# Performance work log

Hardware: AMD Instinct MI355X
Metric: run time of the kernel (lower is better)

Reference implementation:

```python
import jax, jax.numpy as jnp
import numpy as np

D_IN = 1024
D_OUT = 1024
NUM_HEADS = 16
HEAD_DIM = D_OUT // NUM_HEADS


def setup_inputs() -> dict:
    key = jax.random.key(0)
    ks = jax.random.split(key, 6)
    B, S = 2, 2048
    x = jax.random.normal(ks[0], (B, S, D_IN), dtype=jnp.float32)
    # nn.Linear stores weight as [out, in]; y = x @ W.T
    scale_in = 1.0 / np.sqrt(D_IN)
    w_query = jax.random.uniform(ks[1], (D_OUT, D_IN), jnp.float32, -scale_in, scale_in)
    w_key = jax.random.uniform(ks[2], (D_OUT, D_IN), jnp.float32, -scale_in, scale_in)
    w_value = jax.random.uniform(ks[3], (D_OUT, D_IN), jnp.float32, -scale_in, scale_in)
    scale_out = 1.0 / np.sqrt(D_OUT)
    w_out = jax.random.uniform(ks[4], (D_OUT, D_OUT), jnp.float32, -scale_out, scale_out)
    b_out = jax.random.uniform(ks[5], (D_OUT,), jnp.float32, -scale_out, scale_out)
    return {"x": x, "w_query": w_query, "w_key": w_key, "w_value": w_value,
            "w_out": w_out, "b_out": b_out}


def reference(x, w_query, w_key, w_value, w_out, b_out):
    B, S, _ = x.shape
    H, Dh = NUM_HEADS, HEAD_DIM
    # projections (no qkv bias), split heads -> [B, H, S, Dh]
    q = (x @ w_query.T).reshape(B, S, H, Dh).transpose(0, 2, 1, 3)
    k = (x @ w_key.T).reshape(B, S, H, Dh).transpose(0, 2, 1, 3)
    v = (x @ w_value.T).reshape(B, S, H, Dh).transpose(0, 2, 1, 3)
    # explicit [B, H, S, S] scores with causal mask (matches masked_fill(triu,-inf))
    scores = jnp.einsum('bhqd,bhkd->bhqk', q, k)
    causal = jnp.tril(jnp.ones((S, S), dtype=bool))  # True = keep
    scores = jnp.where(causal, scores, -jnp.inf)
    attn = jax.nn.softmax(scores / np.sqrt(Dh).astype(np.float32), axis=-1)
    # dropout p=0.0 -> identity
    ctx = jnp.einsum('bhqk,bhkd->bhqd', attn, v)  # [B, H, S, Dh]
    ctx = ctx.transpose(0, 2, 1, 3).reshape(B, S, H * Dh)
    return ctx @ w_out.T + b_out
```

## Files before the change

### kernel.cpp

```cpp
#include <hip/hip_runtime.h>
#include <hip/hip_bf16.h>

typedef __attribute__((ext_vector_type(8))) short short8;
typedef __attribute__((ext_vector_type(4))) short short4_t;
typedef __attribute__((ext_vector_type(8))) float f32x8;
typedef __attribute__((ext_vector_type(4))) float f32x4;
typedef __attribute__((ext_vector_type(2))) unsigned uint2v;
typedef __attribute__((ext_vector_type(4))) unsigned uint4v;

#define MFMA16(a, b, c) __builtin_amdgcn_mfma_f32_16x16x32_bf16((a), (b), (c), 0, 0, 0)


static __device__ __forceinline__ short f2bf(float f) {
    __hip_bfloat16 h = __float2bfloat16(f);
    return *reinterpret_cast<short*>(&h);
}

static __device__ __forceinline__ unsigned pack2bf(float lo, float hi) {
    return ((unsigned)f2bf(lo) & 0xffffu) | ((unsigned)f2bf(hi) << 16);
}

static __device__ __forceinline__ short8 u4_to_s8(uint4v u) {
    short8 s;
    __builtin_memcpy(&s, &u, 16);
    return s;
}

static __device__ __forceinline__ void g2l16(const void* g, void* l) {
    __builtin_amdgcn_global_load_lds(
        (const __attribute__((address_space(1))) void*)g,
        (__attribute__((address_space(3))) void*)l,
        16, 0, 0);
}

__global__ __launch_bounds__(256) void cvt_kernel(
    const float* __restrict__ x,  const float* __restrict__ wq,
    const float* __restrict__ wk, const float* __restrict__ wv,
    const float* __restrict__ wo, __hip_bfloat16* __restrict__ ws)
{
    const size_t e = ((size_t)blockIdx.x * 256 + threadIdx.x) * 8;
    const float* src;
    __hip_bfloat16* dst;
    size_t off;
    if (e < 4194304)      { src = x;  dst = ws + 16777216; off = e; }
    else if (e < 5242880) { src = wq; dst = ws + 20971520; off = e - 4194304; }
    else if (e < 6291456) { src = wk; dst = ws + 20971520 + 1048576; off = e - 5242880; }
    else if (e < 7340032) { src = wv; dst = ws + 20971520 + 2097152; off = e - 6291456; }
    else                  { src = wo; dst = ws + 24117248; off = e - 7340032; }

    f32x8 v = *reinterpret_cast<const f32x8*>(src + off);
    short8 o;
#pragma unroll
    for (int j = 0; j < 8; ++j) o[j] = f2bf(v[j]);
    *reinterpret_cast<short8*>(reinterpret_cast<short*>(dst) + off) = o;
}

__global__ __launch_bounds__(256) void qkv_gemm_kernel(
    const __hip_bfloat16* __restrict__ xbf_,
    const __hip_bfloat16* __restrict__ wqkv_,
    __hip_bfloat16* __restrict__ qkv_out)
{
    const int bid = blockIdx.x;
    const int xcd = bid & 7, kb = bid >> 3;
    const int mBlk = xcd * 4 + (kb / 24);
    const int nBlk = kb % 24;

    const int tid  = threadIdx.x;
    const int lane = tid & 63;
    const int wid  = tid >> 6;
    const int l16  = lane & 15;
    const int lhi  = lane >> 4;
    const int wr = wid >> 1, wc = wid & 1;

    const short* A = reinterpret_cast<const short*>(xbf_);
    const short* Bm = reinterpret_cast<const short*>(wqkv_);
    const int r0A = mBlk * 128, r0B = nBlk * 128;

    __shared__ __align__(16) short sA[128 * 64];
    __shared__ __align__(16) short sB[128 * 64];

    f32x4 acc[4][4] = {};

    for (int kk = 0; kk < 1024; kk += 64) {
#pragma unroll
        for (int it = 0; it < 4; ++it) {
            const int G = it * 256 + tid;
            const int row = G >> 3, gs = G & 7;
            const int gl = gs ^ (row & 7);
            short* lp = sA + (size_t)(it * 256 + wid * 64) * 8;
            g2l16(A + (size_t)(r0A + row) * 1024 + kk + gl * 8, lp);
        }
#pragma unroll
        for (int it = 0; it < 4; ++it) {
            const int G = it * 256 + tid;
            const int row = G >> 3, gs = G & 7;
            const int gl = gs ^ (row & 7);
            short* lp = sB + (size_t)(it * 256 + wid * 64) * 8;
            g2l16(Bm + (size_t)(r0B + row) * 1024 + kk + gl * 8, lp);
        }
        __syncthreads();

#pragma unroll
        for (int ks = 0; ks < 2; ++ks) {
            short8 a[4], b[4];
#pragma unroll
            for (int i = 0; i < 4; ++i) {
                const int row = wr * 64 + i * 16 + l16;
                const int sg = (ks * 4 + lhi) ^ (row & 7);
                a[i] = *reinterpret_cast<const short8*>(&sA[row * 64 + sg * 8]);
            }
#pragma unroll
            for (int j = 0; j < 4; ++j) {
                const int row = wc * 64 + j * 16 + l16;
                const int sg = (ks * 4 + lhi) ^ (row & 7);
                b[j] = *reinterpret_cast<const short8*>(&sB[row * 64 + sg * 8]);
            }
#pragma unroll
            for (int i = 0; i < 4; ++i)
#pragma unroll
                for (int j = 0; j < 4; ++j)
                    acc[i][j] = MFMA16(a[i], b[j], acc[i][j]);
        }
        __syncthreads();
    }

    const int nTileBase = nBlk * 128 + wc * 64;
    const int mat = (nTileBase >> 10);
    __hip_bfloat16* dst = qkv_out + (size_t)mat * 4194304;
    const int mBase = r0A + wr * 64;

    if (mat < 2) {
        const float qscl = (mat == 0) ? 0.18033688f : 1.0f;
#pragma unroll
        for (int i = 0; i < 4; ++i)
#pragma unroll
            for (int j = 0; j < 4; ++j)
#pragma unroll
                for (int r = 0; r < 4; ++r) {
                    const int mRow = mBase + i * 16 + lhi * 4 + r;
                    const int nCol = (nTileBase + j * 16 + l16) & 1023;
                    const int bb = mRow >> 11, s = mRow & 2047;
                    const int h = nCol >> 6, d = nCol & 63;
                    dst[(((size_t)(bb * 16 + h) * 2048 + s) << 6) + d] =
                        __float2bfloat16(acc[i][j][r] * qscl);
                }
    } else {
#pragma unroll
        for (int i = 0; i < 4; ++i) {
            const int mRow0 = mBase + i * 16 + lhi * 4;
            const int bb = mRow0 >> 11, s0 = mRow0 & 2047;
#pragma unroll
            for (int j = 0; j < 4; ++j) {
                const int nCol = (nTileBase + j * 16 + l16) & 1023;
                const int h = nCol >> 6, d = nCol & 63;
                short4_t v4;
#pragma unroll
                for (int r = 0; r < 4; ++r) v4[r] = f2bf(acc[i][j][r]);
                *reinterpret_cast<short4_t*>(
                    reinterpret_cast<short*>(dst) +
                    (((size_t)(bb * 16 + h) * 64 + d) << 11) + s0) = v4;
            }
        }
    }
}

__global__ __launch_bounds__(256, 4) void attn_kernel(
    const __hip_bfloat16* __restrict__ qkv,
    __hip_bfloat16* __restrict__ ctx)
{
    const int tid  = threadIdx.x;
    const int lane = tid & 63;
    const int wid  = tid >> 6;
    const int l16 = lane & 15;
    const int lhi = lane >> 4;

    const int bid = blockIdx.x;
    const int xcd = bid & 7, idx = bid >> 3;
    const int h4 = idx & 3, tg = idx >> 2;
    const int bh = xcd * 4 + h4;
    const int g  = (tg < 16) ? (31 - tg) : (tg - 16);
    const int qt = g * 4 + wid;
    const int q0 = qt * 16;
    const int ns_blk = g + 1;

    const short* Q  = reinterpret_cast<const short*>(qkv) + (size_t)bh * 131072;
    const short* K  = Q + 4194304;
    const short* Vt = Q + 8388608;

    __shared__ __align__(16) short sK[2][64 * 64];
    __shared__ __align__(16) short sV[2][64 * 64];

    const int bb = bh >> 4, h = bh & 15;
    const int qrow = q0 + l16;
    const int r7 = l16 & 7;

    short8 qf[2];
    qf[0] = *reinterpret_cast<const short8*>(Q + (size_t)qrow * 64 + lhi * 8);
    qf[1] = *reinterpret_cast<const short8*>(Q + (size_t)qrow * 64 + 32 + lhi * 8);

    f32x4 oacc[4] = {};
    float lsum = 0.0f;

    auto stage = [&](int buf, int kv0) {
#pragma unroll
        for (int it = 0; it < 2; ++it) {
            const int G = it * 256 + tid;
            const int row = G >> 3, gs = G & 7;
            const int gl = gs ^ (row & 7);
            g2l16(K + (size_t)(kv0 + row) * 64 + gl * 8, &sK[buf][(size_t)G * 8]);
            g2l16(Vt + (size_t)row * 2048 + kv0 + gl * 8, &sV[buf][(size_t)G * 8]);
        }
    };

    stage(0, 0);
    asm volatile("s_waitcnt vmcnt(0)" ::: "memory");
    __syncthreads();

    int cur = 0;
#pragma unroll 1
    for (int st = 0; st < ns_blk; ++st) {
        const int kv0 = st * 64;
        if (st + 1 < ns_blk) stage(cur ^ 1, kv0 + 64);

        f32x4 sc[4];
#pragma unroll
        for (int nt = 0; nt < 4; ++nt) {
            f32x4 s = {};
#pragma unroll
            for (int ks = 0; ks < 2; ++ks) {
                const int sg = (ks * 4 + lhi) ^ r7;
                short8 kb = *reinterpret_cast<const short8*>(
                    &sK[cur][(nt * 16 + l16) * 64 + sg * 8]);
                s = MFMA16(kb, qf[ks], s);
            }
            sc[nt] = s;
        }

        if (st == ns_blk - 1) {
#pragma unroll
            for (int nt = 0; nt < 4; ++nt) {
                const int kvb = kv0 + nt * 16 + lhi * 4;
#pragma unroll
                for (int r = 0; r < 4; ++r)
                    if (kvb + r > qrow) sc[nt][r] = -1.0e38f;
            }
        }

        unsigned pw[4][2];
#pragma unroll
        for (int nt = 0; nt < 4; ++nt) {
            const float p0 = exp2f(sc[nt][0]);
            const float p1 = exp2f(sc[nt][1]);
            const float p2 = exp2f(sc[nt][2]);
            const float p3 = exp2f(sc[nt][3]);
            lsum += (p0 + p1) + (p2 + p3);
            pw[nt][0] = pack2bf(p0, p1);
            pw[nt][1] = pack2bf(p2, p3);
        }

#pragma unroll
        for (int ks = 0; ks < 2; ++ks) {
            uint4v up;
            up[0] = pw[2 * ks][0];
            up[1] = pw[2 * ks][1];
            up[2] = pw[2 * ks + 1][0];
            up[3] = pw[2 * ks + 1][1];
            short8 pa = u4_to_s8(up);
#pragma unroll
            for (int dt = 0; dt < 4; ++dt) {
                const int row = dt * 16 + l16;
                const int g0 = (ks * 4 + (lhi >> 1)) ^ (row & 7);
                const int g1 = (ks * 4 + 2 + (lhi >> 1)) ^ (row & 7);
                const int sub = (lhi & 1) * 8;
                const char* base = reinterpret_cast<const char*>(&sV[cur][row * 64]);
                uint2v lo  = *reinterpret_cast<const uint2v*>(base + g0 * 16 + sub);
                uint2v hiw = *reinterpret_cast<const uint2v*>(base + g1 * 16 + sub);
                uint4v uv;
                uv[0] = lo[0];  uv[1] = lo[1];
                uv[2] = hiw[0]; uv[3] = hiw[1];
                short8 vb = u4_to_s8(uv);
                oacc[dt] = MFMA16(pa, vb, oacc[dt]);
            }
        }

        asm volatile("s_waitcnt vmcnt(0)" ::: "memory");
        __syncthreads();
        cur ^= 1;
    }

    float rs = lsum;
    rs += __shfl_xor(rs, 16);
    rs += __shfl_xor(rs, 32);
    const float rinvq = 1.0f / rs;
    float rinv[4];
#pragma unroll
    for (int r = 0; r < 4; ++r) rinv[r] = __shfl(rinvq, lhi * 4 + r);

#pragma unroll
    for (int dt = 0; dt < 4; ++dt)
#pragma unroll
        for (int r = 0; r < 4; ++r) {
            const int q = q0 + lhi * 4 + r;
            ctx[((size_t)bb * 2048 + q) * 1024 + h * 64 + dt * 16 + l16] =
                __float2bfloat16(oacc[dt][r] * rinv[r]);
        }
}

__global__ __launch_bounds__(256) void out_gemm_kernel(
    const __hip_bfloat16* __restrict__ ctx,
    const __hip_bfloat16* __restrict__ wobf,
    const float* __restrict__ bo,
    float* __restrict__ out)
{
    const int bid = blockIdx.x;
    const int xcd = bid & 7, kb = bid >> 3;
    const int mBlk = xcd * 4 + (kb >> 3);
    const int nBlk = kb & 7;

    const int tid  = threadIdx.x;
    const int lane = tid & 63;
    const int wid  = tid >> 6;
    const int l16  = lane & 15;
    const int lhi  = lane >> 4;
    const int wr = wid >> 1, wc = wid & 1;

    const short* A = reinterpret_cast<const short*>(ctx);
    const short* Bm = reinterpret_cast<const short*>(wobf);
    const int r0A = mBlk * 128, r0B = nBlk * 128;

    __shared__ __align__(16) short sA[128 * 64];
    __shared__ __align__(16) short sB[128 * 64];

    f32x4 acc[4][4] = {};

    for (int kk = 0; kk < 1024; kk += 64) {
#pragma unroll
        for (int it = 0; it < 4; ++it) {
            const int G = it * 256 + tid;
            const int row = G >> 3, gs = G & 7;
            const int gl = gs ^ (row & 7);
            short* lp = sA + (size_t)(it * 256 + wid * 64) * 8;
            g2l16(A + (size_t)(r0A + row) * 1024 + kk + gl * 8, lp);
        }
#pragma unroll
        for (int it = 0; it < 4; ++it) {
            const int G = it * 256 + tid;
            const int row = G >> 3, gs = G & 7;
            const int gl = gs ^ (row & 7);
            short* lp = sB + (size_t)(it * 256 + wid * 64) * 8;
            g2l16(Bm + (size_t)(r0B + row) * 1024 + kk + gl * 8, lp);
        }
        __syncthreads();

#pragma unroll
        for (int ks = 0; ks < 2; ++ks) {
            short8 a[4], b[4];
#pragma unroll
            for (int i = 0; i < 4; ++i) {
                const int row = wr * 64 + i * 16 + l16;
                const int sg = (ks * 4 + lhi) ^ (row & 7);
                a[i] = *reinterpret_cast<const short8*>(&sA[row * 64 + sg * 8]);
            }
#pragma unroll
            for (int j = 0; j < 4; ++j) {
                const int row = wc * 64 + j * 16 + l16;
                const int sg = (ks * 4 + lhi) ^ (row & 7);
                b[j] = *reinterpret_cast<const short8*>(&sB[row * 64 + sg * 8]);
            }
#pragma unroll
            for (int i = 0; i < 4; ++i)
#pragma unroll
                for (int j = 0; j < 4; ++j)
                    acc[i][j] = MFMA16(a[i], b[j], acc[i][j]);
        }
        __syncthreads();
    }

    const int mBase = r0A + wr * 64;
    const int nBase = r0B + wc * 64;
#pragma unroll
    for (int i = 0; i < 4; ++i)
#pragma unroll
        for (int j = 0; j < 4; ++j)
#pragma unroll
            for (int r = 0; r < 4; ++r) {
                const int mRow = mBase + i * 16 + lhi * 4 + r;
                const int nCol = nBase + j * 16 + l16;
                out[(size_t)mRow * 1024 + nCol] = acc[i][j][r] + bo[nCol];
            }
}

extern "C" void kernel_launch(void* const* d_in, const int* in_sizes, int n_in,
                              void* d_out, int out_size, void* d_ws, size_t ws_size,
                              hipStream_t stream) {
    const float* x  = (const float*)d_in[0];
    const float* wq = (const float*)d_in[1];
    const float* wk = (const float*)d_in[2];
    const float* wv = (const float*)d_in[3];
    const float* wo = (const float*)d_in[4];
    const float* bo = (const float*)d_in[5];

    __hip_bfloat16* ws = (__hip_bfloat16*)d_ws;
    __hip_bfloat16* ctx  = ws + 12582912;
    __hip_bfloat16* xbf  = ws + 16777216;
    __hip_bfloat16* wqkv = ws + 20971520;
    __hip_bfloat16* wobf = ws + 24117248;
    float* out = (float*)d_out;

    cvt_kernel<<<4096, 256, 0, stream>>>(x, wq, wk, wv, wo, ws);
    qkv_gemm_kernel<<<768, 256, 0, stream>>>(xbf, wqkv, ws);
    attn_kernel<<<1024, 256, 0, stream>>>(ws, ctx);
    out_gemm_kernel<<<256, 256, 0, stream>>>(ctx, wobf, bo, out);
}
```

Before: 118.3 us.

## Process two query tiles per wave in attention and vectorize Q/K stores

The attention kernel now gives each wave 32 query rows (two 16-row tiles) instead of 16, so every K/V tile staged in LDS and every fragment read from LDS feeds twice as many MFMAs. Block count is halved to 512 and the occupancy hint drops to 3. Waves whose rows end before the block's last KV tile skip that tile's compute. Separately, the QKV GEMM swaps MFMA operand order for the Q/K outputs so each lane holds 4 contiguous head-dim values and can write them as one 8-byte store instead of scalar stores. The cost is higher register pressure and fewer blocks to balance across CUs.

```diff
diff --git a/kernel.cpp b/kernel.cpp
--- a/kernel.cpp
+++ b/kernel.cpp
@@ -76,6 +76,10 @@
     const short* Bm = reinterpret_cast<const short*>(wqkv_);
     const int r0A = mBlk * 128, r0B = nBlk * 128;
 
+    const int nTileBase = nBlk * 128 + wc * 64;
+    const int mat = (nTileBase >> 10);
+    const bool swp = (mat < 2);
+
     __shared__ __align__(16) short sA[128 * 64];
     __shared__ __align__(16) short sB[128 * 64];
 
@@ -115,35 +119,44 @@
                 const int sg = (ks * 4 + lhi) ^ (row & 7);
                 b[j] = *reinterpret_cast<const short8*>(&sB[row * 64 + sg * 8]);
             }
-#pragma unroll
-            for (int i = 0; i < 4; ++i)
-#pragma unroll
-                for (int j = 0; j < 4; ++j)
-                    acc[i][j] = MFMA16(a[i], b[j], acc[i][j]);
+            if (swp) {
+#pragma unroll
+                for (int i = 0; i < 4; ++i)
+#pragma unroll
+                    for (int j = 0; j < 4; ++j)
+                        acc[i][j] = MFMA16(b[j], a[i], acc[i][j]);
+            } else {
+#pragma unroll
+                for (int i = 0; i < 4; ++i)
+#pragma unroll
+                    for (int j = 0; j < 4; ++j)
+                        acc[i][j] = MFMA16(a[i], b[j], acc[i][j]);
+            }
         }
         __syncthreads();
     }
 
-    const int nTileBase = nBlk * 128 + wc * 64;
-    const int mat = (nTileBase >> 10);
     __hip_bfloat16* dst = qkv_out + (size_t)mat * 4194304;
     const int mBase = r0A + wr * 64;
 
-    if (mat < 2) {
+    if (swp) {
         const float qscl = (mat == 0) ? 0.18033688f : 1.0f;
 #pragma unroll
-        for (int i = 0; i < 4; ++i)
-#pragma unroll
-            for (int j = 0; j < 4; ++j)
-#pragma unroll
-                for (int r = 0; r < 4; ++r) {
-                    const int mRow = mBase + i * 16 + lhi * 4 + r;
-                    const int nCol = (nTileBase + j * 16 + l16) & 1023;
-                    const int bb = mRow >> 11, s = mRow & 2047;
-                    const int h = nCol >> 6, d = nCol & 63;
-                    dst[(((size_t)(bb * 16 + h) * 2048 + s) << 6) + d] =
-                        __float2bfloat16(acc[i][j][r] * qscl);
-                }
+        for (int i = 0; i < 4; ++i) {
+            const int mRow = mBase + i * 16 + l16;
+            const int bb = mRow >> 11, s = mRow & 2047;
+#pragma unroll
+            for (int j = 0; j < 4; ++j) {
+                const int nCol0 = (nTileBase + j * 16 + lhi * 4) & 1023;
+                const int h = nCol0 >> 6, d0 = nCol0 & 63;
+                short4_t v4;
+#pragma unroll
+                for (int r = 0; r < 4; ++r) v4[r] = f2bf(acc[i][j][r] * qscl);
+                *reinterpret_cast<short4_t*>(
+                    reinterpret_cast<short*>(dst) +
+                    (((size_t)(bb * 16 + h) * 2048 + s) << 6) + d0) = v4;
+            }
+        }
     } else {
 #pragma unroll
         for (int i = 0; i < 4; ++i) {
@@ -164,7 +177,7 @@
     }
 }
 
-__global__ __launch_bounds__(256, 4) void attn_kernel(
+__global__ __launch_bounds__(256, 3) void attn_kernel(
     const __hip_bfloat16* __restrict__ qkv,
     __hip_bfloat16* __restrict__ ctx)
 {
@@ -178,10 +191,10 @@
     const int xcd = bid & 7, idx = bid >> 3;
     const int h4 = idx & 3, tg = idx >> 2;
     const int bh = xcd * 4 + h4;
-    const int g  = (tg < 16) ? (31 - tg) : (tg - 16);
-    const int qt = g * 4 + wid;
-    const int q0 = qt * 16;
-    const int ns_blk = g + 1;
+    const int g  = (tg < 8) ? (15 - tg) : (tg - 8);
+    const int q0 = g * 128 + wid * 32;
+    const int sd = (q0 + 31) >> 6;
+    const int ns_blk = 2 * g + 2;
 
     const short* Q  = reinterpret_cast<const short*>(qkv) + (size_t)bh * 131072;
     const short* K  = Q + 4194304;
@@ -191,15 +204,18 @@
     __shared__ __align__(16) short sV[2][64 * 64];
 
     const int bb = bh >> 4, h = bh & 15;
-    const int qrow = q0 + l16;
+    const int qrowA = q0 + l16;
+    const int qrowB = q0 + 16 + l16;
     const int r7 = l16 & 7;
 
-    short8 qf[2];
-    qf[0] = *reinterpret_cast<const short8*>(Q + (size_t)qrow * 64 + lhi * 8);
-    qf[1] = *reinterpret_cast<const short8*>(Q + (size_t)qrow * 64 + 32 + lhi * 8);
-
-    f32x4 oacc[4] = {};
-    float lsum = 0.0f;
+    short8 qfA[2], qfB[2];
+    qfA[0] = *reinterpret_cast<const short8*>(Q + (size_t)qrowA * 64 + lhi * 8);
+    qfA[1] = *reinterpret_cast<const short8*>(Q + (size_t)qrowA * 64 + 32 + lhi * 8);
+    qfB[0] = *reinterpret_cast<const short8*>(Q + (size_t)qrowB * 64 + lhi * 8);
+    qfB[1] = *reinterpret_cast<const short8*>(Q + (size_t)qrowB * 64 + 32 + lhi * 8);
+
+    f32x4 oaccA[4] = {}, oaccB[4] = {};
+    float lsumA = 0.0f, lsumB = 0.0f;
 
     auto stage = [&](int buf, int kv0) {
 #pragma unroll
@@ -222,64 +238,75 @@
         const int kv0 = st * 64;
         if (st + 1 < ns_blk) stage(cur ^ 1, kv0 + 64);
 
-        f32x4 sc[4];
-#pragma unroll
-        for (int nt = 0; nt < 4; ++nt) {
-            f32x4 s = {};
+        if (st <= sd) {
+            f32x4 scA[4], scB[4];
+#pragma unroll
+            for (int nt = 0; nt < 4; ++nt) {
+                f32x4 sa = {}, sb = {};
+#pragma unroll
+                for (int ks = 0; ks < 2; ++ks) {
+                    const int sg = (ks * 4 + lhi) ^ r7;
+                    short8 kb = *reinterpret_cast<const short8*>(
+                        &sK[cur][(nt * 16 + l16) * 64 + sg * 8]);
+                    sa = MFMA16(kb, qfA[ks], sa);
+                    sb = MFMA16(kb, qfB[ks], sb);
+                }
+                scA[nt] = sa;
+                scB[nt] = sb;
+            }
+
+            if (st == sd) {
+#pragma unroll
+                for (int nt = 0; nt < 4; ++nt) {
+                    const int kvb = kv0 + nt * 16 + lhi * 4;
+#pragma unroll
+                    for (int r = 0; r < 4; ++r) {
+                        if (kvb + r > qrowA) scA[nt][r] = -1.0e38f;
+                        if (kvb + r > qrowB) scB[nt][r] = -1.0e38f;
+                    }
+                }
+            }
+
+            unsigned pwA[4][2], pwB[4][2];
+#pragma unroll
+            for (int nt = 0; nt < 4; ++nt) {
+                float a0 = exp2f(scA[nt][0]), a1 = exp2f(scA[nt][1]);
+                float a2 = exp2f(scA[nt][2]), a3 = exp2f(scA[nt][3]);
+                lsumA += (a0 + a1) + (a2 + a3);
+                pwA[nt][0] = pack2bf(a0, a1);
+                pwA[nt][1] = pack2bf(a2, a3);
+                float b0 = exp2f(scB[nt][0]), b1 = exp2f(scB[nt][1]);
+                float b2 = exp2f(scB[nt][2]), b3 = exp2f(scB[nt][3]);
+                lsumB += (b0 + b1) + (b2 + b3);
+                pwB[nt][0] = pack2bf(b0, b1);
+                pwB[nt][1] = pack2bf(b2, b3);
+            }
+
 #pragma unroll
             for (int ks = 0; ks < 2; ++ks) {
-                const int sg = (ks * 4 + lhi) ^ r7;
-                short8 kb = *reinterpret_cast<const short8*>(
-                    &sK[cur][(nt * 16 + l16) * 64 + sg * 8]);
-                s = MFMA16(kb, qf[ks], s);
-            }
-            sc[nt] = s;
-        }
-
-        if (st == ns_blk - 1) {
-#pragma unroll
-            for (int nt = 0; nt < 4; ++nt) {
-                const int kvb = kv0 + nt * 16 + lhi * 4;
-#pragma unroll
-                for (int r = 0; r < 4; ++r)
-                    if (kvb + r > qrow) sc[nt][r] = -1.0e38f;
-            }
-        }
-
-        unsigned pw[4][2];
-#pragma unroll
-        for (int nt = 0; nt < 4; ++nt) {
-            const float p0 = exp2f(sc[nt][0]);
-            const float p1 = exp2f(sc[nt][1]);
-            const float p2 = exp2f(sc[nt][2]);
-            const float p3 = exp2f(sc[nt][3]);
-            lsum += (p0 + p1) + (p2 + p3);
-            pw[nt][0] = pack2bf(p0, p1);
-            pw[nt][1] = pack2bf(p2, p3);
-        }
-
-#pragma unroll
-        for (int ks = 0; ks < 2; ++ks) {
-            uint4v up;
-            up[0] = pw[2 * ks][0];
-            up[1] = pw[2 * ks][1];
-            up[2] = pw[2 * ks + 1][0];
-            up[3] = pw[2 * ks + 1][1];
-            short8 pa = u4_to_s8(up);
-#pragma unroll
-            for (int dt = 0; dt < 4; ++dt) {
-                const int row = dt * 16 + l16;
-                const int g0 = (ks * 4 + (lhi >> 1)) ^ (row & 7);
-                const int g1 = (ks * 4 + 2 + (lhi >> 1)) ^ (row & 7);
-                const int sub = (lhi & 1) * 8;
-                const char* base = reinterpret_cast<const char*>(&sV[cur][row * 64]);
-                uint2v lo  = *reinterpret_cast<const uint2v*>(base + g0 * 16 + sub);
-                uint2v hiw = *reinterpret_cast<const uint2v*>(base + g1 * 16 + sub);
-                uint4v uv;
-                uv[0] = lo[0];  uv[1] = lo[1];
-                uv[2] = hiw[0]; uv[3] = hiw[1];
-                short8 vb = u4_to_s8(uv);
-                oacc[dt] = MFMA16(pa, vb, oacc[dt]);
+                uint4v ua, ub;
+                ua[0] = pwA[2 * ks][0];     ub[0] = pwB[2 * ks][0];
+                ua[1] = pwA[2 * ks][1];     ub[1] = pwB[2 * ks][1];
+                ua[2] = pwA[2 * ks + 1][0]; ub[2] = pwB[2 * ks + 1][0];
+                ua[3] = pwA[2 * ks + 1][1]; ub[3] = pwB[2 * ks + 1][1];
+                short8 paA = u4_to_s8(ua);
+                short8 paB = u4_to_s8(ub);
+#pragma unroll
+                for (int dt = 0; dt < 4; ++dt) {
+                    const int row = dt * 16 + l16;
+                    const int g0 = (ks * 4 + (lhi >> 1)) ^ (row & 7);
+                    const int g1 = (ks * 4 + 2 + (lhi >> 1)) ^ (row & 7);
+                    const int sub = (lhi & 1) * 8;
+                    const char* base = reinterpret_cast<const char*>(&sV[cur][row * 64]);
+                    uint2v lo  = *reinterpret_cast<const uint2v*>(base + g0 * 16 + sub);
+                    uint2v hiw = *reinterpret_cast<const uint2v*>(base + g1 * 16 + sub);
+                    uint4v uv;
+                    uv[0] = lo[0];  uv[1] = lo[1];
+                    uv[2] = hiw[0]; uv[3] = hiw[1];
+                    short8 vb = u4_to_s8(uv);
+                    oaccA[dt] = MFMA16(paA, vb, oaccA[dt]);
+                    oaccB[dt] = MFMA16(paB, vb, oaccB[dt]);
+                }
             }
         }
 
@@ -288,21 +315,31 @@
         cur ^= 1;
     }
 
-    float rs = lsum;
-    rs += __shfl_xor(rs, 16);
-    rs += __shfl_xor(rs, 32);
-    const float rinvq = 1.0f / rs;
-    float rinv[4];
-#pragma unroll
-    for (int r = 0; r < 4; ++r) rinv[r] = __shfl(rinvq, lhi * 4 + r);
+    float rsA = lsumA;
+    rsA += __shfl_xor(rsA, 16);
+    rsA += __shfl_xor(rsA, 32);
+    float rsB = lsumB;
+    rsB += __shfl_xor(rsB, 16);
+    rsB += __shfl_xor(rsB, 32);
+    const float riA = 1.0f / rsA;
+    const float riB = 1.0f / rsB;
+    float rinvA[4], rinvB[4];
+#pragma unroll
+    for (int r = 0; r < 4; ++r) {
+        rinvA[r] = __shfl(riA, lhi * 4 + r);
+        rinvB[r] = __shfl(riB, lhi * 4 + r);
+    }
 
 #pragma unroll
     for (int dt = 0; dt < 4; ++dt)
 #pragma unroll
         for (int r = 0; r < 4; ++r) {
-            const int q = q0 + lhi * 4 + r;
-            ctx[((size_t)bb * 2048 + q) * 1024 + h * 64 + dt * 16 + l16] =
-                __float2bfloat16(oacc[dt][r] * rinv[r]);
+            const int qA = q0 + lhi * 4 + r;
+            ctx[((size_t)bb * 2048 + qA) * 1024 + h * 64 + dt * 16 + l16] =
+                __float2bfloat16(oaccA[dt][r] * rinvA[r]);
+            const int qB = q0 + 16 + lhi * 4 + r;
+            ctx[((size_t)bb * 2048 + qB) * 1024 + h * 64 + dt * 16 + l16] =
+                __float2bfloat16(oaccB[dt][r] * rinvB[r]);
         }
 }
 
@@ -409,6 +446,6 @@
 
     cvt_kernel<<<4096, 256, 0, stream>>>(x, wq, wk, wv, wo, ws);
     qkv_gemm_kernel<<<768, 256, 0, stream>>>(xbf, wqkv, ws);
-    attn_kernel<<<1024, 256, 0, stream>>>(ws, ctx);
+    attn_kernel<<<512, 256, 0, stream>>>(ws, ctx);
     out_gemm_kernel<<<256, 256, 0, stream>>>(ctx, wobf, bo, out);
 }
```

Result: no change. 116.1 us (median of 2 runs) (-1.9%).

## Swap MFMA operands for Q/K stores and single-buffer attention KV for occupancy

Applied to the files above, without the earlier changes.

In the QKV projection GEMM, Q and K tiles now compute the transposed MFMA product, so each lane holds four consecutive head-dim values and can write them as one 8-byte store instead of scattered 2-byte stores. The attention kernel drops the double-buffered K/V shared-memory staging in favour of a single buffer loaded synchronously each step, and raises the launch-bounds occupancy hint from 4 to 6 blocks per CU. This trades away the overlap of global loads with compute for lower LDS use and more resident waves, counting on the higher occupancy to hide memory latency.

```diff
diff --git a/kernel.cpp b/kernel.cpp
--- a/kernel.cpp
+++ b/kernel.cpp
@@ -76,6 +76,10 @@
     const short* Bm = reinterpret_cast<const short*>(wqkv_);
     const int r0A = mBlk * 128, r0B = nBlk * 128;
 
+    const int nTileBase = nBlk * 128 + wc * 64;
+    const int mat = (nTileBase >> 10);
+    const bool swp = (mat < 2);
+
     __shared__ __align__(16) short sA[128 * 64];
     __shared__ __align__(16) short sB[128 * 64];
 
@@ -115,35 +119,44 @@
                 const int sg = (ks * 4 + lhi) ^ (row & 7);
                 b[j] = *reinterpret_cast<const short8*>(&sB[row * 64 + sg * 8]);
             }
-#pragma unroll
-            for (int i = 0; i < 4; ++i)
-#pragma unroll
-                for (int j = 0; j < 4; ++j)
-                    acc[i][j] = MFMA16(a[i], b[j], acc[i][j]);
+            if (swp) {
+#pragma unroll
+                for (int i = 0; i < 4; ++i)
+#pragma unroll
+                    for (int j = 0; j < 4; ++j)
+                        acc[i][j] = MFMA16(b[j], a[i], acc[i][j]);
+            } else {
+#pragma unroll
+                for (int i = 0; i < 4; ++i)
+#pragma unroll
+                    for (int j = 0; j < 4; ++j)
+                        acc[i][j] = MFMA16(a[i], b[j], acc[i][j]);
+            }
         }
         __syncthreads();
     }
 
-    const int nTileBase = nBlk * 128 + wc * 64;
-    const int mat = (nTileBase >> 10);
     __hip_bfloat16* dst = qkv_out + (size_t)mat * 4194304;
     const int mBase = r0A + wr * 64;
 
-    if (mat < 2) {
+    if (swp) {
         const float qscl = (mat == 0) ? 0.18033688f : 1.0f;
 #pragma unroll
-        for (int i = 0; i < 4; ++i)
-#pragma unroll
-            for (int j = 0; j < 4; ++j)
-#pragma unroll
-                for (int r = 0; r < 4; ++r) {
-                    const int mRow = mBase + i * 16 + lhi * 4 + r;
-                    const int nCol = (nTileBase + j * 16 + l16) & 1023;
-                    const int bb = mRow >> 11, s = mRow & 2047;
-                    const int h = nCol >> 6, d = nCol & 63;
-                    dst[(((size_t)(bb * 16 + h) * 2048 + s) << 6) + d] =
-                        __float2bfloat16(acc[i][j][r] * qscl);
-                }
+        for (int i = 0; i < 4; ++i) {
+            const int mRow = mBase + i * 16 + l16;
+            const int bb = mRow >> 11, s = mRow & 2047;
+#pragma unroll
+            for (int j = 0; j < 4; ++j) {
+                const int nCol0 = (nTileBase + j * 16 + lhi * 4) & 1023;
+                const int h = nCol0 >> 6, d0 = nCol0 & 63;
+                short4_t v4;
+#pragma unroll
+                for (int r = 0; r < 4; ++r) v4[r] = f2bf(acc[i][j][r] * qscl);
+                *reinterpret_cast<short4_t*>(
+                    reinterpret_cast<short*>(dst) +
+                    (((size_t)(bb * 16 + h) * 2048 + s) << 6) + d0) = v4;
+            }
+        }
     } else {
 #pragma unroll
         for (int i = 0; i < 4; ++i) {
@@ -164,7 +177,7 @@
     }
 }
 
-__global__ __launch_bounds__(256, 4) void attn_kernel(
+__global__ __launch_bounds__(256, 6) void attn_kernel(
     const __hip_bfloat16* __restrict__ qkv,
     __hip_bfloat16* __restrict__ ctx)
 {
@@ -187,8 +200,8 @@
     const short* K  = Q + 4194304;
     const short* Vt = Q + 8388608;
 
-    __shared__ __align__(16) short sK[2][64 * 64];
-    __shared__ __align__(16) short sV[2][64 * 64];
+    __shared__ __align__(16) short sK[64 * 64];
+    __shared__ __align__(16) short sV[64 * 64];
 
     const int bb = bh >> 4, h = bh & 15;
     const int qrow = q0 + l16;
@@ -201,26 +214,24 @@
     f32x4 oacc[4] = {};
     float lsum = 0.0f;
 
-    auto stage = [&](int buf, int kv0) {
+    auto stage = [&](int kv0) {
 #pragma unroll
         for (int it = 0; it < 2; ++it) {
             const int G = it * 256 + tid;
             const int row = G >> 3, gs = G & 7;
             const int gl = gs ^ (row & 7);
-            g2l16(K + (size_t)(kv0 + row) * 64 + gl * 8, &sK[buf][(size_t)G * 8]);
-            g2l16(Vt + (size_t)row * 2048 + kv0 + gl * 8, &sV[buf][(size_t)G * 8]);
+            g2l16(K + (size_t)(kv0 + row) * 64 + gl * 8, &sK[(size_t)G * 8]);
+            g2l16(Vt + (size_t)row * 2048 + kv0 + gl * 8, &sV[(size_t)G * 8]);
         }
     };
 
-    stage(0, 0);
-    asm volatile("s_waitcnt vmcnt(0)" ::: "memory");
-    __syncthreads();
-
-    int cur = 0;
 #pragma unroll 1
     for (int st = 0; st < ns_blk; ++st) {
         const int kv0 = st * 64;
-        if (st + 1 < ns_blk) stage(cur ^ 1, kv0 + 64);
+
+        stage(kv0);
+        asm volatile("s_waitcnt vmcnt(0)" ::: "memory");
+        __syncthreads();
 
         f32x4 sc[4];
 #pragma unroll
@@ -230,7 +241,7 @@
             for (int ks = 0; ks < 2; ++ks) {
                 const int sg = (ks * 4 + lhi) ^ r7;
                 short8 kb = *reinterpret_cast<const short8*>(
-                    &sK[cur][(nt * 16 + l16) * 64 + sg * 8]);
+                    &sK[(nt * 16 + l16) * 64 + sg * 8]);
                 s = MFMA16(kb, qf[ks], s);
             }
             sc[nt] = s;
@@ -272,7 +283,7 @@
                 const int g0 = (ks * 4 + (lhi >> 1)) ^ (row & 7);
                 const int g1 = (ks * 4 + 2 + (lhi >> 1)) ^ (row & 7);
                 const int sub = (lhi & 1) * 8;
-                const char* base = reinterpret_cast<const char*>(&sV[cur][row * 64]);
+                const char* base = reinterpret_cast<const char*>(&sV[row * 64]);
                 uint2v lo  = *reinterpret_cast<const uint2v*>(base + g0 * 16 + sub);
                 uint2v hiw = *reinterpret_cast<const uint2v*>(base + g1 * 16 + sub);
                 uint4v uv;
@@ -283,9 +294,7 @@
             }
         }
 
-        asm volatile("s_waitcnt vmcnt(0)" ::: "memory");
-        __syncthreads();
-        cur ^= 1;
+        __syncthreads();
     }
 
     float rs = lsum;
```

New measurement: 123.5 us. 4.4% more time.
